# Optimization experiments

Measured on AMD Instinct MI355X. Metric: run time of the kernel, lower is better.

The kernel has to match this reference:

```python
import jax, jax.numpy as jnp
import numpy as np

N_NODES = 50000
N_EDGES = 800000
D_IN = 256
D_HID = 256
D_OUT = 256


def sage_conv(x, src, dst, W_l, b_l, W_r, num_nodes):
    """PyG SAGEConv with mean aggregation: lin_l(mean_{j in N(i)} x_j) + lin_r(x_i)."""
    msg = x[src]  # [E, C] gather of source-node features
    agg = jax.ops.segment_sum(msg, dst, num_segments=num_nodes)  # [N, C]
    cnt = jax.ops.segment_sum(jnp.ones((src.shape[0],), x.dtype), dst,
                              num_segments=num_nodes)
    mean = agg / jnp.maximum(cnt, 1.0)[:, None]  # isolated nodes -> 0
    return mean @ W_l.T + b_l + x @ W_r.T


def setup_inputs() -> dict:
    key = jax.random.key(0)
    ks = jax.random.split(key, 10)
    s = 1.0 / np.sqrt(D_IN)
    x = jax.random.normal(ks[0], (N_NODES, D_IN), dtype=jnp.float32)
    edge_index = jax.random.randint(ks[1], (2, N_EDGES), 0, N_NODES, dtype=jnp.int64)
    mention_index = jax.random.randint(ks[2], (1,), 0, N_NODES, dtype=jnp.int64)
    return {
        "x": x,
        "edge_index": edge_index,
        "mention_index": mention_index,
        "W1_l": jax.random.uniform(ks[3], (D_HID, D_IN), jnp.float32, -s, s),
        "b1_l": jnp.zeros((D_HID,), jnp.float32),
        "W1_r": jax.random.uniform(ks[4], (D_HID, D_IN), jnp.float32, -s, s),
        "W2_l": jax.random.uniform(ks[5], (D_OUT, D_HID), jnp.float32, -s, s),
        "b2_l": jnp.zeros((D_OUT,), jnp.float32),
        "W2_r": jax.random.uniform(ks[6], (D_OUT, D_HID), jnp.float32, -s, s),
    }


def reference(x, edge_index, mention_index, W1_l, b1_l, W1_r, W2_l, b2_l, W2_r):
    src, dst = edge_index[0], edge_index[1]
    h = jax.nn.relu(sage_conv(x, src, dst, W1_l, b1_l, W1_r, N_NODES))
    h = sage_conv(h, src, dst, W2_l, b2_l, W2_r, N_NODES)
    # dropout in the original is a no-op (result discarded)
    logits = (h[mention_index] * h).sum(axis=1)  # [N]
    z = jax.nn.softmax(logits, axis=0)
    return z
```

## Files before the change

kernel.cpp:

```cpp
#include <hip/hip_runtime.h>
#include <math.h>

#define N_NODES 50000
#define N_EDGES 800000
#define D 256
#define K2 512
#define M_PAD 50048
#define BM 128
#define BN 256
#define BK 32
#define SCAN_B 196
#define SPX_B 12500
#define SPB_B 128
#define CNT_B 3125

typedef __attribute__((ext_vector_type(8))) short short8;
typedef __attribute__((ext_vector_type(8))) unsigned short ushort8;
typedef __attribute__((ext_vector_type(4))) float floatx4;

#if defined(__has_builtin)
#if __has_builtin(__builtin_amdgcn_cvt_pk_f32_fp8) && __has_builtin(__builtin_amdgcn_cvt_pk_fp8_f32)
#define HAVE_HW_FP8 1
#endif
#endif
#ifndef HAVE_HW_FP8
#define HAVE_HW_FP8 0
#endif

__device__ __forceinline__ unsigned short bf16_rn(float f) {
    union { float f; unsigned u; } a; a.f = f;
    unsigned r = a.u + 0x7FFF + ((a.u >> 16) & 1);
    return (unsigned short)(r >> 16);
}
__device__ __forceinline__ float bf16_to_f(unsigned short h) {
    union { unsigned u; float f; } a; a.u = ((unsigned)h) << 16;
    return a.f;
}
__device__ __forceinline__ void load_lds16(const void* g, void* lds) {
    __builtin_amdgcn_global_load_lds((const __attribute__((address_space(1))) void*)g,
                                     (__attribute__((address_space(3))) void*)lds, 16, 0, 0);
}

#if HAVE_HW_FP8
#define FP8_ACC_SCALE 1.0f
__device__ __forceinline__ unsigned int fp8x4_enc(float4 v) {
    int p = 0;
    p = __builtin_amdgcn_cvt_pk_fp8_f32(v.x, v.y, p, 0);
    p = __builtin_amdgcn_cvt_pk_fp8_f32(v.z, v.w, p, 1);
    return (unsigned int)p;
}
__device__ __forceinline__ void fp8x4_acc(unsigned int w, float* acc) {
    auto p0 = __builtin_amdgcn_cvt_pk_f32_fp8((int)w, 0);
    auto p1 = __builtin_amdgcn_cvt_pk_f32_fp8((int)w, 1);
    acc[0] += p0[0]; acc[1] += p0[1]; acc[2] += p1[0]; acc[3] += p1[1];
}
#else
#define FP8_ACC_SCALE 0x1p120f
__device__ __forceinline__ unsigned char fp8_enc1(float f) {
    union { float f; unsigned u; } a; a.f = f;
    unsigned s = (a.u >> 24) & 0x80;
    int e = (int)((a.u >> 23) & 0xFF);
    unsigned m = a.u & 0x7FFFFF;
    unsigned mr = m + 0x7FFFF + ((m >> 20) & 1);
    if (mr >= 0x800000) { mr = 0; e += 1; }
    int e8 = e - 120;
    if (e8 <= 0) return (unsigned char)s;
    if (e8 > 15) { e8 = 15; mr = 6u << 20; }
    unsigned char r = (unsigned char)(s | (e8 << 3) | (mr >> 20));
    if ((r & 0x7F) == 0x7F) r -= 1;
    return r;
}
__device__ __forceinline__ unsigned int fp8x4_enc(float4 v) {
    return (unsigned)fp8_enc1(v.x) | ((unsigned)fp8_enc1(v.y) << 8) |
           ((unsigned)fp8_enc1(v.z) << 16) | ((unsigned)fp8_enc1(v.w) << 24);
}
__device__ __forceinline__ void fp8x4_acc(unsigned int w, float* acc) {
    #pragma unroll
    for (int k = 0; k < 4; k++) {
        unsigned b = (w >> (8 * k)) & 0xFF;
        union { unsigned u; float f; } a;
        a.u = ((b & 0x80) << 24) | ((b & 0x7F) << 20);
        acc[k] += a.f;
    }
}
#endif

__global__ __launch_bounds__(256) void k_init(const float* __restrict__ x,
                                              const float* __restrict__ Wl,
                                              const float* __restrict__ Wr,
                                              const int* __restrict__ dst,
                                              unsigned short* __restrict__ Ahi,
                                              unsigned short* __restrict__ Alo,
                                              unsigned short* __restrict__ Bhi,
                                              unsigned short* __restrict__ Blo,
                                              unsigned char* __restrict__ Xf8,
                                              int* __restrict__ deg) {
    int b = blockIdx.x;
    if (b < SPX_B) {
        int t = b * 256 + threadIdx.x;
        int m = t >> 6, j = (t & 63) * 4;
        float4 v = *(const float4*)&x[(size_t)m * D + j];
        ushort4 hi, lo;
        hi.x = bf16_rn(v.x); lo.x = bf16_rn(v.x - bf16_to_f(hi.x));
        hi.y = bf16_rn(v.y); lo.y = bf16_rn(v.y - bf16_to_f(hi.y));
        hi.z = bf16_rn(v.z); lo.z = bf16_rn(v.z - bf16_to_f(hi.z));
        hi.w = bf16_rn(v.w); lo.w = bf16_rn(v.w - bf16_to_f(hi.w));
        *(ushort4*)&Ahi[(size_t)m * K2 + 256 + j] = hi;
        *(ushort4*)&Alo[(size_t)m * K2 + 256 + j] = lo;
        *(unsigned int*)&Xf8[(size_t)m * D + j] = fp8x4_enc(v);
    } else if (b < SPX_B + SPB_B) {
        int t = (b - SPX_B) * 256 + threadIdx.x;
        int n = t >> 7, k = (t & 127) * 4;
        const float* srcp = (k < 256) ? &Wl[(size_t)n * 256 + k] : &Wr[(size_t)n * 256 + k - 256];
        float4 v = *(const float4*)srcp;
        ushort4 hi, lo;
        hi.x = bf16_rn(v.x); lo.x = bf16_rn(v.x - bf16_to_f(hi.x));
        hi.y = bf16_rn(v.y); lo.y = bf16_rn(v.y - bf16_to_f(hi.y));
        hi.z = bf16_rn(v.z); lo.z = bf16_rn(v.z - bf16_to_f(hi.z));
        hi.w = bf16_rn(v.w); lo.w = bf16_rn(v.w - bf16_to_f(hi.w));
        *(ushort4*)&Bhi[(size_t)n * K2 + k] = hi;
        *(ushort4*)&Blo[(size_t)n * K2 + k] = lo;
    } else {
        int e = (b - SPX_B - SPB_B) * 256 + threadIdx.x;
        if (e < N_EDGES) atomicAdd(&deg[dst[e]], 1);
    }
}

__global__ void k_scan1(const int* __restrict__ deg, int* __restrict__ bsum) {
    __shared__ int red[256];
    int b = blockIdx.x, t = threadIdx.x;
    int i = b * 256 + t;
    red[t] = (i < N_NODES) ? deg[i] : 0;
    __syncthreads();
    for (int o = 128; o; o >>= 1) {
        if (t < o) red[t] += red[t + o];
        __syncthreads();
    }
    if (t == 0) bsum[b] = red[0];
}

__global__ void k_scan23(const int* __restrict__ deg, const int* __restrict__ bsum,
                         int* __restrict__ cursor) {
    __shared__ int sh[256];
    int b = blockIdx.x, t = threadIdx.x;
    sh[t] = (t < SCAN_B) ? bsum[t] : 0;
    __syncthreads();
    for (int o = 1; o < 256; o <<= 1) {
        int v = (t >= o) ? sh[t - o] : 0;
        __syncthreads();
        sh[t] += v;
        __syncthreads();
    }
    int boff = (b == 0) ? 0 : sh[b - 1];
    __syncthreads();
    int i = b * 256 + t;
    int v = (i < N_NODES) ? deg[i] : 0;
    sh[t] = v;
    __syncthreads();
    for (int o = 1; o < 256; o <<= 1) {
        int val = (t >= o) ? sh[t - o] : 0;
        __syncthreads();
        sh[t] += val;
        __syncthreads();
    }
    if (i < N_NODES) cursor[i] = boff + sh[t] - v;
}

__global__ void k_bucket(const int* __restrict__ src, const int* __restrict__ dst,
                         int* __restrict__ cursor, int* __restrict__ csr_src) {
    int e = blockIdx.x * blockDim.x + threadIdx.x;
    if (e >= N_EDGES) return;
    int pos = atomicAdd(&cursor[dst[e]], 1);
    csr_src[pos] = src[e];
}

__global__ __launch_bounds__(256) void k_agg(const int* __restrict__ cursor,
                                             const int* __restrict__ deg,
                                             const int* __restrict__ csr,
                                             const unsigned char* __restrict__ Xf8,
                                             unsigned short* __restrict__ Ahi,
                                             unsigned short* __restrict__ Alo) {
    int node = blockIdx.x * 4 + (threadIdx.x >> 6);
    int lane = threadIdx.x & 63;
    if (node >= N_NODES) return;
    int d = deg[node], end = cursor[node], start = end - d;
    int h = lane >> 5;
    int col = (lane & 31) * 8;
    const unsigned char* Xb = Xf8 + col;
    float acc0[8] = {}, acc1[8] = {}, acc2[8] = {}, acc3[8] = {};
    int j = start;
    for (; j + 16 <= end; j += 16) {
        int i0 = csr[j + h],      i1 = csr[j + 2 + h],  i2 = csr[j + 4 + h],  i3 = csr[j + 6 + h];
        int i4 = csr[j + 8 + h],  i5 = csr[j + 10 + h], i6 = csr[j + 12 + h], i7 = csr[j + 14 + h];
        uint2 v0 = *(const uint2*)&Xb[(size_t)i0 * D];
        uint2 v1 = *(const uint2*)&Xb[(size_t)i1 * D];
        uint2 v2 = *(const uint2*)&Xb[(size_t)i2 * D];
        uint2 v3 = *(const uint2*)&Xb[(size_t)i3 * D];
        uint2 v4 = *(const uint2*)&Xb[(size_t)i4 * D];
        uint2 v5 = *(const uint2*)&Xb[(size_t)i5 * D];
        uint2 v6 = *(const uint2*)&Xb[(size_t)i6 * D];
        uint2 v7 = *(const uint2*)&Xb[(size_t)i7 * D];
        fp8x4_acc(v0.x, acc0); fp8x4_acc(v0.y, acc0 + 4);
        fp8x4_acc(v1.x, acc1); fp8x4_acc(v1.y, acc1 + 4);
        fp8x4_acc(v2.x, acc2); fp8x4_acc(v2.y, acc2 + 4);
        fp8x4_acc(v3.x, acc3); fp8x4_acc(v3.y, acc3 + 4);
        fp8x4_acc(v4.x, acc0); fp8x4_acc(v4.y, acc0 + 4);
        fp8x4_acc(v5.x, acc1); fp8x4_acc(v5.y, acc1 + 4);
        fp8x4_acc(v6.x, acc2); fp8x4_acc(v6.y, acc2 + 4);
        fp8x4_acc(v7.x, acc3); fp8x4_acc(v7.y, acc3 + 4);
    }
    if (j + 8 <= end) {
        int i0 = csr[j + h], i1 = csr[j + 2 + h], i2 = csr[j + 4 + h], i3 = csr[j + 6 + h];
        uint2 v0 = *(const uint2*)&Xb[(size_t)i0 * D];
        uint2 v1 = *(const uint2*)&Xb[(size_t)i1 * D];
        uint2 v2 = *(const uint2*)&Xb[(size_t)i2 * D];
        uint2 v3 = *(const uint2*)&Xb[(size_t)i3 * D];
        fp8x4_acc(v0.x, acc0); fp8x4_acc(v0.y, acc0 + 4);
        fp8x4_acc(v1.x, acc1); fp8x4_acc(v1.y, acc1 + 4);
        fp8x4_acc(v2.x, acc2); fp8x4_acc(v2.y, acc2 + 4);
        fp8x4_acc(v3.x, acc3); fp8x4_acc(v3.y, acc3 + 4);
        j += 8;
    }
    if (j + 4 <= end) {
        int i0 = csr[j + h], i1 = csr[j + 2 + h];
        uint2 v0 = *(const uint2*)&Xb[(size_t)i0 * D];
        uint2 v1 = *(const uint2*)&Xb[(size_t)i1 * D];
        fp8x4_acc(v0.x, acc0); fp8x4_acc(v0.y, acc0 + 4);
        fp8x4_acc(v1.x, acc1); fp8x4_acc(v1.y, acc1 + 4);
        j += 4;
    }
    if (j + 2 <= end) {
        int i0 = csr[j + h];
        uint2 v0 = *(const uint2*)&Xb[(size_t)i0 * D];
        fp8x4_acc(v0.x, acc0); fp8x4_acc(v0.y, acc0 + 4);
        j += 2;
    }
    if (j < end && h == 0) {
        int i0 = csr[j];
        uint2 v0 = *(const uint2*)&Xb[(size_t)i0 * D];
        fp8x4_acc(v0.x, acc0); fp8x4_acc(v0.y, acc0 + 4);
    }
    float inv = FP8_ACC_SCALE / fmaxf((float)d, 1.0f);
    ushort8 hi, lo;
    #pragma unroll
    for (int k = 0; k < 8; k++) {
        float a = (acc0[k] + acc1[k]) + (acc2[k] + acc3[k]);
        a += __shfl_xor(a, 32);
        float m = a * inv;
        hi[k] = bf16_rn(m);
        lo[k] = bf16_rn(m - bf16_to_f(hi[k]));
    }
    if (h == 0) {
        *(ushort8*)&Ahi[(size_t)node * K2 + col] = hi;
        *(ushort8*)&Alo[(size_t)node * K2 + col] = lo;
    }
}

__global__ __launch_bounds__(256) void k_small(const int* __restrict__ mention,
                                               const int* __restrict__ deg,
                                               const int* __restrict__ cursor,
                                               const int* __restrict__ csr,
                                               const float* __restrict__ x,
                                               const float* __restrict__ W1l,
                                               const float* __restrict__ W1r,
                                               const float* __restrict__ b1,
                                               float* __restrict__ h1m) {
    int m = mention[0];
    int dm = min(deg[m], 95);
    int slot = blockIdx.x;
    if (slot > dm) return;
    int startm = cursor[m] - deg[m];
    int node = (slot == 0) ? m : csr[startm + slot - 1];
    __shared__ float smean[D], sx[D];
    int t = threadIdx.x;
    int d = deg[node], end = cursor[node], start = end - d;
    float a = 0.f;
    for (int j = start; j < end; j++) a += x[(size_t)csr[j] * D + t];
    smean[t] = a / fmaxf((float)d, 1.0f);
    sx[t] = x[(size_t)node * D + t];
    __syncthreads();
    float z = b1[t];
    const float* wl = &W1l[(size_t)t * D];
    const float* wr = &W1r[(size_t)t * D];
    for (int k = 0; k < D; k += 4) {
        float4 a4 = *(const float4*)&wl[k];
        float4 b4 = *(const float4*)&wr[k];
        z += smean[k] * a4.x + smean[k + 1] * a4.y + smean[k + 2] * a4.z + smean[k + 3] * a4.w
           + sx[k] * b4.x + sx[k + 1] * b4.y + sx[k + 2] * b4.z + sx[k + 3] * b4.w;
    }
    h1m[(size_t)slot * D + t] = fmaxf(z, 0.f);
}

__global__ __launch_bounds__(256) void k_v(const int* __restrict__ mention,
                                           const int* __restrict__ deg,
                                           const float* __restrict__ h1m,
                                           const float* __restrict__ W2l,
                                           const float* __restrict__ W2r,
                                           const float* __restrict__ b2,
                                           float* __restrict__ v) {
    __shared__ float sm[D], sh[D];
    int m = mention[0];
    int dm = min(deg[m], 95);
    int t = threadIdx.x;
    float a = 0.f;
    for (int j = 1; j <= dm; j++) a += h1m[(size_t)j * D + t];
    sm[t] = a / fmaxf((float)deg[m], 1.0f);
    sh[t] = h1m[t];
    __syncthreads();
    int o = t >> 4, p = t & 15;
    int row = blockIdx.x * 16 + o;
    const float* wl = &W2l[(size_t)row * D];
    const float* wr = &W2r[(size_t)row * D];
    float acc = 0.f;
    int k0 = p * 16;
    #pragma unroll
    for (int k = k0; k < k0 + 16; k += 4) {
        float4 a4 = *(const float4*)&wl[k];
        float4 b4 = *(const float4*)&wr[k];
        acc += sm[k] * a4.x + sm[k + 1] * a4.y + sm[k + 2] * a4.z + sm[k + 3] * a4.w
             + sh[k] * b4.x + sh[k + 1] * b4.y + sh[k + 2] * b4.z + sh[k + 3] * b4.w;
    }
    #pragma unroll
    for (int off = 1; off < 16; off <<= 1) acc += __shfl_xor(acc, off);
    if (p == 0) v[row] = acc + b2[row];
}

__global__ __launch_bounds__(256) void k_u(const float* __restrict__ W2l,
                                           const float* __restrict__ W2r,
                                           const float* __restrict__ b2,
                                           const float* __restrict__ v,
                                           float* __restrict__ u,
                                           float* __restrict__ cout) {
    __shared__ float sv[D];
    __shared__ float r1[4][64], r2[4][64], red[256];
    int t = threadIdx.x;
    sv[t] = v[t];
    __syncthreads();
    int lane = t & 63, p = t >> 6;
    int col = blockIdx.x * 64 + lane;
    float a1 = 0.f, a2 = 0.f;
    for (int n = p; n < D; n += 4) {
        float vv = sv[n];
        a1 += W2l[(size_t)n * D + col] * vv;
        a2 += W2r[(size_t)n * D + col] * vv;
    }
    r1[p][lane] = a1; r2[p][lane] = a2;
    __syncthreads();
    if (p == 0) {
        u[col] = r1[0][lane] + r1[1][lane] + r1[2][lane] + r1[3][lane];
        u[D + col] = r2[0][lane] + r2[1][lane] + r2[2][lane] + r2[3][lane];
    }
    if (blockIdx.x == 0) {
        red[t] = b2[t] * sv[t];
        __syncthreads();
        for (int o = 128; o; o >>= 1) {
            if (t < o) red[t] += red[t + o];
            __syncthreads();
        }
        if (t == 0) cout[0] = red[0];
    }
}

__global__ __launch_bounds__(512, 4)
void k_gemm_fused(const unsigned short* __restrict__ Ahi,
                  const unsigned short* __restrict__ Alo,
                  const unsigned short* __restrict__ Bhi,
                  const unsigned short* __restrict__ Blo,
                  const float* __restrict__ bias,
                  const float* __restrict__ u,
                  float* __restrict__ s,
                  float* __restrict__ t_) {
    __shared__ unsigned short sA[2][BM * BK];
    __shared__ unsigned short sB[2][BN * BK];
    __shared__ float sred[BM], tred[BM];
    int tid = threadIdx.x;
    int br = blockIdx.x;
    int lane = tid & 63, wv = tid >> 6;
    int wm = (wv >> 2) * 64, wn = (wv & 3) * 64;
    int q = lane >> 4, r = lane & 15;

    float biasv[4], u1v[4], u2v[4];
    #pragma unroll
    for (int nt = 0; nt < 4; nt++) {
        int gc = wn + nt * 16 + r;
        biasv[nt] = bias[gc];
        u1v[nt] = u[gc];
        u2v[nt] = u[256 + gc];
    }
    if (tid < BM) { sred[tid] = 0.f; tred[tid] = 0.f; }

    floatx4 acc[4][4] = {};

    const size_t arow0 = (size_t)br * BM;
    int seg = lane & 3;
    int rl16 = lane >> 2;

    for (int kt = 0; kt < K2 / BK; kt++) {
        {
            int rloc = wv * 16 + rl16;
            size_t gA = (arow0 + rloc) * (size_t)K2 + kt * BK + seg * 8;
            int ldsoff = (wv * 16) * BK;
            load_lds16(Ahi + gA, &sA[0][ldsoff]);
            load_lds16(Alo + gA, &sA[1][ldsoff]);
        }
        #pragma unroll
        for (int t = 0; t < 2; t++) {
            int rloc = wv * 32 + t * 16 + rl16;
            size_t gB = (size_t)rloc * K2 + kt * BK + seg * 8;
            int ldsoff = (wv * 32 + t * 16) * BK;
            load_lds16(Bhi + gB, &sB[0][ldsoff]);
            load_lds16(Blo + gB, &sB[1][ldsoff]);
        }
        __syncthreads();
        short8 ah[4], al[4], bh[4], bl[4];
        #pragma unroll
        for (int i = 0; i < 4; i++) {
            ah[i] = *(const short8*)&sA[0][(wm + i * 16 + r) * BK + q * 8];
            al[i] = *(const short8*)&sA[1][(wm + i * 16 + r) * BK + q * 8];
            bh[i] = *(const short8*)&sB[0][(wn + i * 16 + r) * BK + q * 8];
            bl[i] = *(const short8*)&sB[1][(wn + i * 16 + r) * BK + q * 8];
        }
        #pragma unroll
        for (int mt = 0; mt < 4; mt++)
            #pragma unroll
            for (int nt = 0; nt < 4; nt++) {
                acc[mt][nt] = __builtin_amdgcn_mfma_f32_16x16x32_bf16(ah[mt], bh[nt], acc[mt][nt], 0, 0, 0);
                acc[mt][nt] = __builtin_amdgcn_mfma_f32_16x16x32_bf16(ah[mt], bl[nt], acc[mt][nt], 0, 0, 0);
                acc[mt][nt] = __builtin_amdgcn_mfma_f32_16x16x32_bf16(al[mt], bh[nt], acc[mt][nt], 0, 0, 0);
            }
        __syncthreads();
    }

    #pragma unroll
    for (int mt = 0; mt < 4; mt++) {
        #pragma unroll
        for (int reg = 0; reg < 4; reg++) {
            float sacc = 0.f, tacc = 0.f;
            #pragma unroll
            for (int nt = 0; nt < 4; nt++) {
                float h = fmaxf(acc[mt][nt][reg] + biasv[nt], 0.f);
                sacc += h * u1v[nt];
                tacc += h * u2v[nt];
            }
            #pragma unroll
            for (int off = 1; off < 16; off <<= 1) {
                sacc += __shfl_xor(sacc, off);
                tacc += __shfl_xor(tacc, off);
            }
            if (r == 0) {
                int row = wm + mt * 16 + q * 4 + reg;
                atomicAdd(&sred[row], sacc);
                atomicAdd(&tred[row], tacc);
            }
        }
    }
    __syncthreads();
    if (tid < BM) {
        size_t grow = arow0 + tid;
        if (grow < N_NODES) {
            s[grow] = sred[tid];
            t_[grow] = tred[tid];
        }
    }
}

__global__ __launch_bounds__(256) void k_logits_sm1(const int* __restrict__ deg,
                                                    const int* __restrict__ cursor,
                                                    const int* __restrict__ csr,
                                                    const float* __restrict__ s,
                                                    const float* __restrict__ t_,
                                                    const float* __restrict__ cptr,
                                                    float* __restrict__ logits,
                                                    float* __restrict__ pmax,
                                                    float* __restrict__ psum) {
    __shared__ float red[256];
    int b = blockIdx.x, t = threadIdx.x;
    int i = b * 256 + t;
    float lg = -INFINITY;
    if (i < N_NODES) {
        int d = deg[i];
        int end = cursor[i];
        int start = end - d;
        float sum = 0.f;
        for (int j = start; j < end; j++) sum += s[csr[j]];
        lg = sum / fmaxf((float)d, 1.0f) + t_[i] + cptr[0];
        logits[i] = lg;
    }
    red[t] = lg;
    __syncthreads();
    for (int o = 128; o; o >>= 1) {
        if (t < o) red[t] = fmaxf(red[t], red[t + o]);
        __syncthreads();
    }
    float mb = red[0];
    __syncthreads();
    red[t] = (i < N_NODES) ? __expf(lg - mb) : 0.f;
    __syncthreads();
    for (int o = 128; o; o >>= 1) {
        if (t < o) red[t] += red[t + o];
        __syncthreads();
    }
    if (t == 0) { pmax[b] = mb; psum[b] = red[0]; }
}

__global__ __launch_bounds__(256) void k_sm23(const float* __restrict__ logits,
                                              const float* __restrict__ pmax,
                                              const float* __restrict__ psum,
                                              float* __restrict__ out) {
    __shared__ float rm[256], rs[256];
    int b = blockIdx.x, t = threadIdx.x;
    float m = (t < SCAN_B) ? pmax[t] : -INFINITY;
    rm[t] = m;
    __syncthreads();
    for (int o = 128; o; o >>= 1) {
        if (t < o) rm[t] = fmaxf(rm[t], rm[t + o]);
        __syncthreads();
    }
    float g = rm[0];
    __syncthreads();
    rs[t] = (t < SCAN_B) ? psum[t] * __expf(m - g) : 0.f;
    __syncthreads();
    for (int o = 128; o; o >>= 1) {
        if (t < o) rs[t] += rs[t + o];
        __syncthreads();
    }
    float inv = 1.0f / rs[0];
    int i = b * 256 + t;
    if (i < N_NODES) out[i] = __expf(logits[i] - g) * inv;
}

extern "C" void kernel_launch(void* const* d_in, const int* in_sizes, int n_in,
                              void* d_out, int out_size, void* d_ws, size_t ws_size,
                              hipStream_t stream) {
    const float* x   = (const float*)d_in[0];
    const int*   ei  = (const int*)d_in[1];
    const int*   src = ei;
    const int*   dst = ei + N_EDGES;
    const int*   mention = (const int*)d_in[2];
    const float* W1l = (const float*)d_in[3];
    const float* b1  = (const float*)d_in[4];
    const float* W1r = (const float*)d_in[5];
    const float* W2l = (const float*)d_in[6];
    const float* b2  = (const float*)d_in[7];
    const float* W2r = (const float*)d_in[8];

    char* w = (char*)d_ws;
    unsigned short* Ahi = (unsigned short*)w;  w += (size_t)M_PAD * K2 * 2;
    unsigned short* Alo = (unsigned short*)w;  w += (size_t)M_PAD * K2 * 2;
    unsigned short* Bhi = (unsigned short*)w;  w += (size_t)256 * K2 * 2;
    unsigned short* Blo = (unsigned short*)w;  w += (size_t)256 * K2 * 2;
    unsigned char* Xf8 = (unsigned char*)w;    w += (size_t)N_NODES * D;
    float* s     = (float*)w;  w += (size_t)N_NODES * 4;
    float* t_    = (float*)w;  w += (size_t)N_NODES * 4;
    int* deg     = (int*)w;    w += (size_t)N_NODES * 4;
    float* logit = (float*)w;  w += (size_t)N_NODES * 4;
    float* h1m   = (float*)w;  w += (size_t)96 * D * 4;
    float* vbuf  = (float*)w;  w += D * 4;
    float* u     = (float*)w;  w += 2 * D * 4;
    float* c     = (float*)w;  w += 16;
    float* pmax  = (float*)w;  w += 256 * 4;
    float* psum  = (float*)w;  w += 256 * 4;
    int* cursor  = (int*)w;    w += (size_t)N_NODES * 4;
    int* bsum    = (int*)w;    w += 256 * 4;
    int* csr     = (int*)w;    w += (size_t)N_EDGES * 4;

    hipMemsetAsync(deg, 0, (size_t)N_NODES * sizeof(int), stream);

    k_init  <<<SPX_B + SPB_B + CNT_B, 256, 0, stream>>>(x, W1l, W1r, dst,
                                                        Ahi, Alo, Bhi, Blo, Xf8, deg);
    k_scan1 <<<SCAN_B, 256, 0, stream>>>(deg, bsum);
    k_scan23<<<SCAN_B, 256, 0, stream>>>(deg, bsum, cursor);
    k_bucket<<<(N_EDGES + 255) / 256, 256, 0, stream>>>(src, dst, cursor, csr);

    k_agg   <<<(N_NODES + 3) / 4, 256, 0, stream>>>(cursor, deg, csr, Xf8, Ahi, Alo);

    k_small <<<96, 256, 0, stream>>>(mention, deg, cursor, csr, x, W1l, W1r, b1, h1m);
    k_v     <<<16, 256, 0, stream>>>(mention, deg, h1m, W2l, W2r, b2, vbuf);
    k_u     <<<4, 256, 0, stream>>>(W2l, W2r, b2, vbuf, u, c);

    k_gemm_fused<<<M_PAD / BM, 512, 0, stream>>>(Ahi, Alo, Bhi, Blo, b1, u, s, t_);

    k_logits_sm1<<<SCAN_B, 256, 0, stream>>>(deg, cursor, csr, s, t_, c, logit, pmax, psum);
    k_sm23  <<<SCAN_B, 256, 0, stream>>>(logit, pmax, psum, (float*)d_out);
}
```

Baseline: 350.7 us.

## Drop low-part split for aggregated half of GEMM and shrink tile to 64 rows

The aggregation kernel now writes only a single bf16 value for the mean features, with no residual low part. The fused GEMM runs the first K half (aggregated features) as a single bf16 MFMA pass and keeps the three-pass hi/lo split only for the second half (x features). The block tile shrinks from 128 to 64 rows with 4 waves, each covering 64 output columns, so there are twice as many blocks. This cuts MFMA work, Alo writes and Alo/Blo loads for half of K, at the cost of lower precision on the mean-aggregation term.

```diff
diff --git a/kernel.cpp b/kernel.cpp
--- a/kernel.cpp
+++ b/kernel.cpp
@@ -6,7 +6,7 @@
 #define D 256
 #define K2 512
 #define M_PAD 50048
-#define BM 128
+#define BM 64
 #define BN 256
 #define BK 32
 #define SCAN_B 196
@@ -178,8 +178,7 @@
                                              const int* __restrict__ deg,
                                              const int* __restrict__ csr,
                                              const unsigned char* __restrict__ Xf8,
-                                             unsigned short* __restrict__ Ahi,
-                                             unsigned short* __restrict__ Alo) {
+                                             unsigned short* __restrict__ Ahi) {
     int node = blockIdx.x * 4 + (threadIdx.x >> 6);
     int lane = threadIdx.x & 63;
     if (node >= N_NODES) return;
@@ -241,18 +240,15 @@
         fp8x4_acc(v0.x, acc0); fp8x4_acc(v0.y, acc0 + 4);
     }
     float inv = FP8_ACC_SCALE / fmaxf((float)d, 1.0f);
-    ushort8 hi, lo;
+    ushort8 hi;
     #pragma unroll
     for (int k = 0; k < 8; k++) {
         float a = (acc0[k] + acc1[k]) + (acc2[k] + acc3[k]);
         a += __shfl_xor(a, 32);
-        float m = a * inv;
-        hi[k] = bf16_rn(m);
-        lo[k] = bf16_rn(m - bf16_to_f(hi[k]));
+        hi[k] = bf16_rn(a * inv);
     }
     if (h == 0) {
         *(ushort8*)&Ahi[(size_t)node * K2 + col] = hi;
-        *(ushort8*)&Alo[(size_t)node * K2 + col] = lo;
     }
 }
 
@@ -361,7 +357,7 @@
     }
 }
 
-__global__ __launch_bounds__(512, 4)
+__global__ __launch_bounds__(256, 4)
 void k_gemm_fused(const unsigned short* __restrict__ Ahi,
                   const unsigned short* __restrict__ Alo,
                   const unsigned short* __restrict__ Bhi,
@@ -376,7 +372,7 @@
     int tid = threadIdx.x;
     int br = blockIdx.x;
     int lane = tid & 63, wv = tid >> 6;
-    int wm = (wv >> 2) * 64, wn = (wv & 3) * 64;
+    int wn = wv * 64;
     int q = lane >> 4, r = lane & 15;
 
     float biasv[4], u1v[4], u2v[4];
@@ -395,28 +391,51 @@
     int seg = lane & 3;
     int rl16 = lane >> 2;
 
-    for (int kt = 0; kt < K2 / BK; kt++) {
+    for (int kt = 0; kt < 8; kt++) {
         {
-            int rloc = wv * 16 + rl16;
-            size_t gA = (arow0 + rloc) * (size_t)K2 + kt * BK + seg * 8;
-            int ldsoff = (wv * 16) * BK;
-            load_lds16(Ahi + gA, &sA[0][ldsoff]);
-            load_lds16(Alo + gA, &sA[1][ldsoff]);
+            size_t gA = (arow0 + wv * 16 + rl16) * (size_t)K2 + kt * BK + seg * 8;
+            load_lds16(Ahi + gA, &sA[0][(wv * 16) * BK]);
         }
         #pragma unroll
-        for (int t = 0; t < 2; t++) {
-            int rloc = wv * 32 + t * 16 + rl16;
+        for (int t = 0; t < 4; t++) {
+            int rloc = wv * 64 + t * 16 + rl16;
             size_t gB = (size_t)rloc * K2 + kt * BK + seg * 8;
-            int ldsoff = (wv * 32 + t * 16) * BK;
-            load_lds16(Bhi + gB, &sB[0][ldsoff]);
-            load_lds16(Blo + gB, &sB[1][ldsoff]);
+            load_lds16(Bhi + gB, &sB[0][(wv * 64 + t * 16) * BK]);
+        }
+        __syncthreads();
+        short8 ah[4], bh[4];
+        #pragma unroll
+        for (int i = 0; i < 4; i++) {
+            ah[i] = *(const short8*)&sA[0][(i * 16 + r) * BK + q * 8];
+            bh[i] = *(const short8*)&sB[0][(wn + i * 16 + r) * BK + q * 8];
+        }
+        #pragma unroll
+        for (int mt = 0; mt < 4; mt++)
+            #pragma unroll
+            for (int nt = 0; nt < 4; nt++)
+                acc[mt][nt] = __builtin_amdgcn_mfma_f32_16x16x32_bf16(ah[mt], bh[nt], acc[mt][nt], 0, 0, 0);
+        __syncthreads();
+    }
+
+    for (int kt = 8; kt < 16; kt++) {
+        {
+            size_t gA = (arow0 + wv * 16 + rl16) * (size_t)K2 + kt * BK + seg * 8;
+            load_lds16(Ahi + gA, &sA[0][(wv * 16) * BK]);
+            load_lds16(Alo + gA, &sA[1][(wv * 16) * BK]);
+        }
+        #pragma unroll
+        for (int t = 0; t < 4; t++) {
+            int rloc = wv * 64 + t * 16 + rl16;
+            size_t gB = (size_t)rloc * K2 + kt * BK + seg * 8;
+            load_lds16(Bhi + gB, &sB[0][(wv * 64 + t * 16) * BK]);
+            load_lds16(Blo + gB, &sB[1][(wv * 64 + t * 16) * BK]);
         }
         __syncthreads();
         short8 ah[4], al[4], bh[4], bl[4];
         #pragma unroll
         for (int i = 0; i < 4; i++) {
-            ah[i] = *(const short8*)&sA[0][(wm + i * 16 + r) * BK + q * 8];
-            al[i] = *(const short8*)&sA[1][(wm + i * 16 + r) * BK + q * 8];
+            ah[i] = *(const short8*)&sA[0][(i * 16 + r) * BK + q * 8];
+            al[i] = *(const short8*)&sA[1][(i * 16 + r) * BK + q * 8];
             bh[i] = *(const short8*)&sB[0][(wn + i * 16 + r) * BK + q * 8];
             bl[i] = *(const short8*)&sB[1][(wn + i * 16 + r) * BK + q * 8];
         }
@@ -448,7 +467,7 @@
                 tacc += __shfl_xor(tacc, off);
             }
             if (r == 0) {
-                int row = wm + mt * 16 + q * 4 + reg;
+                int row = mt * 16 + q * 4 + reg;
                 atomicAdd(&sred[row], sacc);
                 atomicAdd(&tred[row], tacc);
             }
@@ -572,13 +591,13 @@
     k_scan23<<<SCAN_B, 256, 0, stream>>>(deg, bsum, cursor);
     k_bucket<<<(N_EDGES + 255) / 256, 256, 0, stream>>>(src, dst, cursor, csr);
 
-    k_agg   <<<(N_NODES + 3) / 4, 256, 0, stream>>>(cursor, deg, csr, Xf8, Ahi, Alo);
+    k_agg   <<<(N_NODES + 3) / 4, 256, 0, stream>>>(cursor, deg, csr, Xf8, Ahi);
 
     k_small <<<96, 256, 0, stream>>>(mention, deg, cursor, csr, x, W1l, W1r, b1, h1m);
     k_v     <<<16, 256, 0, stream>>>(mention, deg, h1m, W2l, W2r, b2, vbuf);
     k_u     <<<4, 256, 0, stream>>>(W2l, W2r, b2, vbuf, u, c);
 
-    k_gemm_fused<<<M_PAD / BM, 512, 0, stream>>>(Ahi, Alo, Bhi, Blo, b1, u, s, t_);
+    k_gemm_fused<<<M_PAD / BM, 256, 0, stream>>>(Ahi, Alo, Bhi, Blo, b1, u, s, t_);
 
     k_logits_sm1<<<SCAN_B, 256, 0, stream>>>(deg, cursor, csr, s, t_, c, logit, pmax, psum);
     k_sm23  <<<SCAN_B, 256, 0, stream>>>(logit, pmax, psum, (float*)d_out);
```

Measured after the change: 343.6 us. 1.02x faster.
